# Kernel optimization log

Measured on AMD Instinct MI355X. Metric: run time of the kernel, lower is better.

Reference implementation:

```python
import jax, jax.numpy as jnp
import numpy as np

B, C, H, W = 4, 32, 64, 64
K = 3
HEADS = 8
SF = 4
D = C * K * K          # 288, unfold token dim
E = D // 2             # 144, reduced dim
DH = E // HEADS        # 18, head dim
SCALE = DH ** -0.5
N = H * W              # 4096 tokens


def unfold(x):
    # x: (B,C,H,W) -> (B, C*K*K, H*W), torch.nn.Unfold ordering (c, kh, kw)
    xp = jnp.pad(x, ((0, 0), (0, 0), (1, 1), (1, 1)))
    patches = jnp.stack([xp[:, :, i:i + H, j:j + W] for i in range(K) for j in range(K)], axis=2)
    return patches.reshape(x.shape[0], C * K * K, H * W)


def fold(cols):
    # inverse of unfold: scatter-add overlapping patches back, crop padding
    b = cols.shape[0]
    y = cols.reshape(b, C, K, K, H, W)
    out = jnp.zeros((b, C, H + 2, W + 2), cols.dtype)
    for i in range(K):
        for j in range(K):
            out = out.at[:, :, i:i + H, j:j + W].add(y[:, :, i, j])
    return out[:, :, 1:-1, 1:-1]


def layernorm_cols(cols, g, b):
    # LayerNorm over D applied on (B,N,D) view, returned as (B,D,N)
    xt = cols.transpose(0, 2, 1)
    mu = xt.mean(-1, keepdims=True)
    var = xt.var(-1, keepdims=True)
    y = (xt - mu) / jnp.sqrt(var + 1e-5) * g + b
    return y.transpose(0, 2, 1)


def emha(x, wr, br, wqkv, we, be):
    # x: (B, D, N)
    b, _, n_tok = x.shape
    xr = jnp.einsum('bdn,ed->ben', x, wr) + br[None, :, None]   # Conv1d k=1 reduction
    t = xr.transpose(0, 2, 1)                                   # (B,N,E)
    qkv = t @ wqkv.T                                            # Linear, no bias
    q, k, v = jnp.split(qkv, 3, axis=-1)
    n = n_tok // SF

    def rs(a):
        return a.reshape(b, n_tok, HEADS, DH).transpose(0, 2, 1, 3).reshape(b, HEADS, SF, n, DH)

    q, k, v = rs(q), rs(k), rs(v)
    attn = jax.nn.softmax(jnp.einsum('bhsnd,bhsmd->bhsnm', q, k) * SCALE, axis=-1)
    o = jnp.einsum('bhsnm,bhsmd->bhsnd', attn, v)
    o = o.reshape(b, HEADS, n_tok, DH).transpose(0, 2, 1, 3).reshape(b, n_tok, E).transpose(0, 2, 1)
    return jnp.einsum('ben,fe->bfn', o, we) + be[None, :, None]  # Conv1d k=1 expansion


def conv3x3(x, w, b):
    y = jax.lax.conv_general_dilated(x, w, (1, 1), ((1, 1), (1, 1)),
                                     dimension_numbers=('NCHW', 'OIHW', 'NCHW'))
    return y + b[None, :, None, None]


def setup_inputs() -> dict:
    key = jax.random.key(0)
    ks = jax.random.split(key, 20)
    s = 0.02
    inp = {
        'x': jax.random.normal(ks[0], (B, C, H, W), jnp.float32),
        'ln_g': jnp.ones((D,), jnp.float32),
        'ln_b': jnp.zeros((D,), jnp.float32),
        'conv_w': jax.random.normal(ks[1], (C, C, 3, 3), jnp.float32) * s,
        'conv_b': jnp.zeros((C,), jnp.float32),
    }
    for i in range(3):
        k0, k1, k2 = jax.random.split(ks[2 + i], 3)
        inp[f'wr{i+1}'] = jax.random.normal(k0, (E, D), jnp.float32) * s
        inp[f'br{i+1}'] = jnp.zeros((E,), jnp.float32)
        inp[f'wqkv{i+1}'] = jax.random.normal(k1, (3 * E, E), jnp.float32) * s
        inp[f'we{i+1}'] = jax.random.normal(k2, (D, E), jnp.float32) * s
        inp[f'be{i+1}'] = jnp.zeros((D,), jnp.float32)
    return inp


def reference(x, ln_g, ln_b, conv_w, conv_b,
              wr1, br1, wqkv1, we1, be1,
              wr2, br2, wqkv2, we2, be2,
              wr3, br3, wqkv3, we3, be3):
    t = x
    for (wr, br, wqkv, we, be) in ((wr1, br1, wqkv1, we1, be1),
                                   (wr2, br2, wqkv2, we2, be2),
                                   (wr3, br3, wqkv3, we3, be3)):
        cols = unfold(t)
        cols_n = layernorm_cols(cols, ln_g, ln_b)
        cols = emha(cols_n, wr, br, wqkv, we, be) + cols
        t = fold(cols)
    return x + jax.nn.elu(conv3x3(t, conv_w, conv_b))
```

## Files before the change

### kernel.cpp

```cpp
#include <hip/hip_runtime.h>
#include <math.h>

#define BN 4
#define CC 32
#define HH 64
#define WW 64
#define DD 288
#define EE 144
#define NTOK 4096
#define SCALE_F 0.2357022603955158f
#define QSCALE  0.3401074286f
#define QKST 384
#define MQKV 528

typedef __bf16 bf16x8 __attribute__((ext_vector_type(8)));
typedef float floatx4 __attribute__((ext_vector_type(4)));
typedef unsigned short u16x8 __attribute__((ext_vector_type(8)));

__device__ __forceinline__ unsigned short f2bf(float x) {
    unsigned int u = __float_as_uint(x);
    u += 0x7fffu + ((u >> 16) & 1u);
    return (unsigned short)(u >> 16);
}
__device__ __forceinline__ float bf2f(unsigned short s) {
    return __uint_as_float(((unsigned int)s) << 16);
}
__device__ __forceinline__ unsigned int pack_bf_trunc(float a, float b) {
    return __builtin_amdgcn_perm(__float_as_uint(b), __float_as_uint(a), 0x07060302u);
}

__global__ void precompute_k(const float* __restrict__ wr0, const float* __restrict__ br0,
                             const float* __restrict__ wr1, const float* __restrict__ br1,
                             const float* __restrict__ wr2, const float* __restrict__ br2,
                             const float* __restrict__ g,  const float* __restrict__ lb,
                             unsigned short* __restrict__ wg_bf, float* __restrict__ wgsum,
                             float* __restrict__ wbeta)
{
    int l = blockIdx.x;
    int e = threadIdx.x;
    const float* wr = (l == 0) ? wr0 : ((l == 1) ? wr1 : wr2);
    const float* br = (l == 0) ? br0 : ((l == 1) ? br1 : br2);
    float sg = 0.f, sb = 0.f;
    for (int d = 0; d < DD; ++d) {
        float w = wr[e * DD + d];
        float wgv = w * g[d];
        wg_bf[((size_t)l * EE + e) * DD + d] = f2bf(wgv);
        sg += wgv;
        sb += w * lb[d];
    }
    wgsum[l * EE + e] = sg;
    wbeta[l * EE + e] = sb + br[e];
}

__global__ __launch_bounds__(256) void convw_k(
    const float* __restrict__ wqkv0, const float* __restrict__ wqkv1, const float* __restrict__ wqkv2,
    const float* __restrict__ we0,   const float* __restrict__ we1,   const float* __restrict__ we2,
    unsigned short* __restrict__ wqkv_bf, unsigned short* __restrict__ we_bf)
{
    int idx = blockIdx.x * 256 + threadIdx.x;
    const int T1 = 3 * MQKV * 160;
    const int T2 = 3 * 288 * 160;
    if (idx < T1) {
        int l = idx / (MQKV * 160), r = idx % (MQKV * 160);
        int m = r / 160, k = r % 160;
        const float* w = (l == 0) ? wqkv0 : ((l == 1) ? wqkv1 : wqkv2);
        float v = 0.f;
        if (k < 144) {
            if (m < 192) {
                int h = m / 24, j = m % 24;
                if (j < 18) v = w[(h * 18 + j) * 144 + k] * QSCALE;
            } else if (m < 384) {
                int mm = m - 192, h = mm / 24, j = mm % 24;
                if (j < 18) v = w[(144 + h * 18 + j) * 144 + k];
            } else {
                v = w[(288 + (m - 384)) * 144 + k];
            }
        }
        wqkv_bf[idx] = f2bf(v);
    } else if (idx < T1 + T2) {
        int j = idx - T1;
        int l = j / (288 * 160), r = j % (288 * 160);
        int m = r / 160, k = r % 160;
        const float* w = (l == 0) ? we0 : ((l == 1) ? we1 : we2);
        we_bf[j] = (k < 144) ? f2bf(w[m * 144 + k]) : 0;
    }
}

__global__ __launch_bounds__(256) void unfold_k(const float* __restrict__ t,
    unsigned short* __restrict__ colsT,
    float* __restrict__ mu, float* __restrict__ rstd)
{
    __shared__ float red1[4][64], red2[4][64];
    int tid = threadIdx.x;
    int lane = tid & 63, cpart = tid >> 6;
    int b = blockIdx.x >> 6, nc = blockIdx.x & 63;
    int n = nc * 64 + lane;
    int h = n >> 6, w = n & 63;
    const float* tb = t + (size_t)b * CC * HH * WW;
    unsigned short loc[72];
    float s1 = 0.f, s2 = 0.f;
    #pragma unroll
    for (int c8 = 0; c8 < 8; ++c8) {
        int c = cpart * 8 + c8;
        const float* tc = tb + (size_t)c * 4096;
        #pragma unroll
        for (int i = 0; i < 3; ++i) {
            int hr = h + i - 1;
            bool rok = ((unsigned)hr < 64u);
            #pragma unroll
            for (int j = 0; j < 3; ++j) {
                int wc = w + j - 1;
                bool ok = rok && ((unsigned)wc < 64u);
                float v = ok ? tc[hr * 64 + wc] : 0.f;
                loc[c8 * 9 + i * 3 + j] = f2bf(v);
                s1 += v;
                s2 = fmaf(v, v, s2);
            }
        }
    }
    unsigned short* ct = colsT + ((size_t)b * NTOK + n) * 288 + cpart * 72;
    #pragma unroll
    for (int u = 0; u < 9; ++u)
        *(u16x8*)&ct[u * 8] = *(const u16x8*)&loc[u * 8];
    red1[cpart][lane] = s1;
    red2[cpart][lane] = s2;
    __syncthreads();
    if (tid < 64) {
        float a = red1[0][tid] + red1[1][tid] + red1[2][tid] + red1[3][tid];
        float q = red2[0][tid] + red2[1][tid] + red2[2][tid] + red2[3][tid];
        float m = a * (1.f / 288.f);
        float var = q * (1.f / 288.f) - m * m;
        int nn = nc * 64 + tid;
        mu[b * NTOK + nn] = m;
        rstd[b * NTOK + nn] = rsqrtf(var + 1e-5f);
    }
}

template<int K, int MODE, int NYB>
__global__ __launch_bounds__(256) void mgemm_k(
    const unsigned short* __restrict__ A, const unsigned short* __restrict__ Bt, int BST,
    unsigned short* __restrict__ Ct, unsigned short* __restrict__ Cv,
    const float* __restrict__ mu, const float* __restrict__ rstd,
    const float* __restrict__ wgsum, const float* __restrict__ wbeta,
    const float* __restrict__ bias)
{
    constexpr int NT = 64;
    __shared__ unsigned short Ts[64 * 56];
    int flat = blockIdx.x;
    int g  = (flat / (8 * NYB)) * 8 + (flat & 7);
    int jm = (flat % (8 * NYB)) >> 3;
    int n0 = (g & 63) * NT;
    int bI = g >> 6;
    int m0 = jm * 48;
    int tid = threadIdx.x;
    int wv = tid >> 6, lane = tid & 63;
    int l15 = lane & 15, l4 = lane >> 4;

    const unsigned short* Arow = A + (size_t)(m0 + l15) * K + l4 * 8;
    const unsigned short* Brow = Bt + ((size_t)bI * NTOK + n0 + wv * 16 + l15) * BST + l4 * 8;

    floatx4 acc[3];
    acc[0] = acc[1] = acc[2] = (floatx4){0.f, 0.f, 0.f, 0.f};

    #pragma unroll
    for (int ks = 0; ks < K / 32; ++ks) {
        bf16x8 bfr = *(const bf16x8*)(Brow + ks * 32);
        #pragma unroll
        for (int mi = 0; mi < 3; ++mi) {
            bf16x8 af = *(const bf16x8*)(Arow + (size_t)mi * 16 * K + ks * 32);
            acc[mi] = __builtin_amdgcn_mfma_f32_16x16x32_bf16(af, bfr, acc[mi], 0, 0, 0);
        }
    }

    int n_l = wv * 16 + l15;

    if (MODE == 2) {
        #pragma unroll
        for (int mi = 0; mi < 3; ++mi)
            #pragma unroll
            for (int r = 0; r < 4; ++r) {
                int m_l = mi * 16 + l4 * 4 + r;
                Ts[m_l * 72 + n_l] = f2bf(acc[mi][r] + bias[m0 + m_l]);
            }
        __syncthreads();
        for (int u = tid; u < 48 * 8; u += 256) {
            int row = u >> 3, seg = u & 7;
            unsigned short* dst = Ct + ((size_t)bI * DD + m0 + row) * NTOK + n0 + seg * 8;
            *(u16x8*)dst = *(const u16x8*)&Ts[row * 72 + seg * 8];
        }
    } else {
        bool vpath = (MODE == 0) && (m0 >= 384);
        float muv = 0.f, rsv = 0.f;
        if (MODE == 1) {
            int n_g = n0 + n_l;
            muv = mu[bI * NTOK + n_g];
            rsv = rstd[bI * NTOK + n_g];
        }
        #pragma unroll
        for (int mi = 0; mi < 3; ++mi)
            #pragma unroll
            for (int r = 0; r < 4; ++r) {
                int m_l = mi * 16 + l4 * 4 + r;
                float v = acc[mi][r];
                if (MODE == 1) v = rsv * (v - muv * wgsum[m0 + m_l]) + wbeta[m0 + m_l];
                if (!vpath) Ts[n_l * 56 + m_l] = f2bf(v);
                else        Ts[m_l * 72 + n_l] = f2bf(v);
            }
        __syncthreads();
        if (!vpath) {
            const int CTS = (MODE == 1) ? 160 : QKST;
            if (tid < 128) {
                int row = tid >> 1, half = tid & 1;
                unsigned short* dst = Ct + ((size_t)bI * NTOK + n0 + row) * CTS + m0 + half * 24;
                const unsigned short* src = &Ts[row * 56 + half * 24];
                #pragma unroll
                for (int u = 0; u < 3; ++u)
                    *(u16x8*)&dst[u * 8] = *(const u16x8*)&src[u * 8];
                if (MODE == 1 && m0 == 96) {
                    u16x8 z = (u16x8)0;
                    *(u16x8*)(Ct + ((size_t)bI * NTOK + n0 + row) * 160 + 144 + half * 8) = z;
                }
            }
        } else {
            for (int u = tid; u < 48 * 8; u += 256) {
                int row = u >> 3, seg = u & 7;
                unsigned short* dst = Cv + ((size_t)bI * EE + (m0 - 384) + row) * NTOK + n0 + seg * 8;
                *(u16x8*)dst = *(const u16x8*)&Ts[row * 72 + seg * 8];
            }
        }
    }
}

__global__ __launch_bounds__(256) void attn_k2(const unsigned short* __restrict__ qkT,
                                               const unsigned short* __restrict__ vF,
                                               unsigned short* __restrict__ oT)
{
    __shared__ unsigned short Ks[128 * 40];
    __shared__ unsigned short Vs[32 * 136];
    __shared__ unsigned short Ps[4 * 32 * 72];

    int blk = blockIdx.x;
    int bhs = blk & 127;
    int qc  = blk >> 7;
    int b = bhs >> 5, h = (bhs >> 2) & 7, s = bhs & 3;
    int tid  = threadIdx.x;
    int wv   = tid >> 6;
    int lane = tid & 63;
    int l15 = lane & 15, l4 = lane >> 4;
    int q0 = qc * 128;
    int tokbase = s * 1024;

    const unsigned short* qkb = qkT + (size_t)b * NTOK * QKST;

    if (tid < 128) {
        u16x8 z = (u16x8)0;
        *(u16x8*)&Ks[tid * 40 + 24] = z;
    } else {
        for (int v = tid - 128; v < 14 * 16; v += 128) {
            int d = 18 + (v >> 4), seg = v & 15;
            unsigned short val = (d == 31) ? (unsigned short)0x3F80 : (unsigned short)0;
            u16x8 vv = (u16x8)val;
            *(u16x8*)&Vs[d * 136 + seg * 8] = vv;
        }
    }

    bf16x8 qf[2];
    #pragma unroll
    for (int ni = 0; ni < 2; ++ni) {
        u16x8 raw = *(const u16x8*)(qkb + (size_t)(tokbase + q0 + wv * 32 + ni * 16 + l15) * QKST
                                    + 24 * h + l4 * 8);
        if (l4 == 3) raw = (u16x8)0;
        qf[ni] = *(bf16x8*)&raw;
    }

    floatx4 oacc[2][2];
    #pragma unroll
    for (int i = 0; i < 2; ++i)
        #pragma unroll
        for (int j = 0; j < 2; ++j)
            oacc[i][j] = (floatx4){0.f, 0.f, 0.f, 0.f};

    unsigned short* Pw = &Ps[wv * 32 * 72];

    u16x8 preg[3];
    int vb = tid - 128;
    bool v3 = (vb < 32);
    if (tid < 128) {
        const unsigned short* src = qkb + (size_t)(tokbase + tid) * QKST + 192 + 24 * h;
        preg[0] = *(const u16x8*)&src[0];
        preg[1] = *(const u16x8*)&src[8];
        preg[2] = *(const u16x8*)&src[16];
    } else {
        const unsigned short* vbb = vF + (size_t)b * EE * NTOK + tokbase;
        #pragma unroll
        for (int u = 0; u < 3; ++u) {
            int idx = vb + u * 128;
            if (u < 2 || v3) {
                int d = idx >> 4, seg = idx & 15;
                preg[u] = *(const u16x8*)(vbb + (size_t)(h * 18 + d) * NTOK + seg * 8);
            }
        }
    }

    for (int c0 = 0; c0 < 1024; c0 += 128) {
        __syncthreads();
        if (tid < 128) {
            unsigned short* dk = &Ks[tid * 40];
            *(u16x8*)&dk[0]  = preg[0];
            *(u16x8*)&dk[8]  = preg[1];
            *(u16x8*)&dk[16] = preg[2];
        } else {
            #pragma unroll
            for (int u = 0; u < 3; ++u) {
                int idx = vb + u * 128;
                if (u < 2 || v3) {
                    int d = idx >> 4, seg = idx & 15;
                    *(u16x8*)&Vs[d * 136 + seg * 8] = preg[u];
                }
            }
        }
        int cn = c0 + 128;
        if (cn < 1024) {
            if (tid < 128) {
                const unsigned short* src = qkb + (size_t)(tokbase + cn + tid) * QKST + 192 + 24 * h;
                preg[0] = *(const u16x8*)&src[0];
                preg[1] = *(const u16x8*)&src[8];
                preg[2] = *(const u16x8*)&src[16];
            } else {
                const unsigned short* vbb = vF + (size_t)b * EE * NTOK + tokbase + cn;
                #pragma unroll
                for (int u = 0; u < 3; ++u) {
                    int idx = vb + u * 128;
                    if (u < 2 || v3) {
                        int d = idx >> 4, seg = idx & 15;
                        preg[u] = *(const u16x8*)(vbb + (size_t)(h * 18 + d) * NTOK + seg * 8);
                    }
                }
            }
        }
        __syncthreads();

        #pragma unroll
        for (int sub = 0; sub < 2; ++sub) {
            bf16x8 kf[4];
            #pragma unroll
            for (int mi = 0; mi < 4; ++mi)
                kf[mi] = *(const bf16x8*)&Ks[(sub * 64 + mi * 16 + l15) * 40 + l4 * 8];

            floatx4 sacc[4][2];
            #pragma unroll
            for (int mi = 0; mi < 4; ++mi)
                #pragma unroll
                for (int ni = 0; ni < 2; ++ni) {
                    floatx4 z = (floatx4){0.f, 0.f, 0.f, 0.f};
                    sacc[mi][ni] = __builtin_amdgcn_mfma_f32_16x16x32_bf16(kf[mi], qf[ni], z, 0, 0, 0);
                }

            #pragma unroll
            for (int mi = 0; mi < 4; ++mi)
                #pragma unroll
                for (int ni = 0; ni < 2; ++ni) {
                    int ql   = ni * 16 + l15;
                    int tokb = mi * 16 + l4 * 4;
                    unsigned int lo = pack_bf_trunc(exp2f(sacc[mi][ni][0]), exp2f(sacc[mi][ni][1]));
                    unsigned int hi = pack_bf_trunc(exp2f(sacc[mi][ni][2]), exp2f(sacc[mi][ni][3]));
                    uint2 pk = make_uint2(lo, hi);
                    *(uint2*)&Pw[ql * 72 + tokb] = pk;
                }

            #pragma unroll
            for (int ks = 0; ks < 2; ++ks) {
                bf16x8 pf[2], vf[2];
                pf[0] = *(const bf16x8*)&Pw[(     l15) * 72 + ks * 32 + l4 * 8];
                pf[1] = *(const bf16x8*)&Pw[(16 + l15) * 72 + ks * 32 + l4 * 8];
                vf[0] = *(const bf16x8*)&Vs[(     l15) * 136 + sub * 64 + ks * 32 + l4 * 8];
                vf[1] = *(const bf16x8*)&Vs[(16 + l15) * 136 + sub * 64 + ks * 32 + l4 * 8];
                #pragma unroll
                for (int mi = 0; mi < 2; ++mi)
                    #pragma unroll
                    for (int nd = 0; nd < 2; ++nd)
                        oacc[mi][nd] = __builtin_amdgcn_mfma_f32_16x16x32_bf16(pf[mi], vf[nd], oacc[mi][nd], 0, 0, 0);
            }
        }
    }

    float* fO = (float*)Pw;
    #pragma unroll
    for (int mi = 0; mi < 2; ++mi)
        #pragma unroll
        for (int r = 0; r < 4; ++r) {
            float lsum = __shfl(oacc[mi][1][r], (lane & 48) | 15, 64);
            float inv  = 1.f / lsum;
            int ql = mi * 16 + l4 * 4 + r;
            fO[ql * 33 + l15] = oacc[mi][0][r] * inv;
            if (l15 < 2) fO[ql * 33 + 16 + l15] = oacc[mi][1][r] * inv;
        }

    {
        int q = lane & 31, dh = lane >> 5;
        size_t rowi = (size_t)b * NTOK + tokbase + q0 + wv * 32 + q;
        unsigned short* orow = oT + rowi * 160 + h * 18;
        for (int i = dh; i < 9; i += 2) {
            float a  = fO[q * 33 + 2 * i];
            float bb = fO[q * 33 + 2 * i + 1];
            *(unsigned int*)&orow[2 * i] = (unsigned)f2bf(a) | ((unsigned)f2bf(bb) << 16);
        }
        if (h == 7) {
            u16x8 z = (u16x8)0;
            *(u16x8*)(oT + rowi * 160 + 144 + dh * 8) = z;
        }
    }
}

__global__ __launch_bounds__(256) void fold_k(const unsigned short* __restrict__ cols,
                                              const float* __restrict__ tprev,
                                              float* __restrict__ t)
{
    int idx = blockIdx.x * 256 + threadIdx.x;
    int w = idx & 63;
    int h = (idx >> 6) & 63;
    int c = (idx >> 12) & 31;
    int b = idx >> 17;
    const unsigned short* cb = cols + (size_t)b * DD * NTOK + (size_t)c * 9 * NTOK;
    float sum = 0.f;
    #pragma unroll
    for (int i = 0; i < 3; ++i) {
        int hs = h + 1 - i;
        if ((unsigned)hs < 64u) {
            #pragma unroll
            for (int j = 0; j < 3; ++j) {
                int ws_ = w + 1 - j;
                if ((unsigned)ws_ < 64u)
                    sum += bf2f(cb[(size_t)(i * 3 + j) * NTOK + hs * 64 + ws_]);
            }
        }
    }
    int ch = (h == 0 || h == 63) ? 2 : 3;
    int cw_ = (w == 0 || w == 63) ? 2 : 3;
    t[idx] = sum + (float)(ch * cw_) * tprev[idx];
}

__global__ __launch_bounds__(256) void conv_k(const float* __restrict__ t,
    const float* __restrict__ cw, const float* __restrict__ cbias,
    const float* __restrict__ x, float* __restrict__ out)
{
    __shared__ float wsh[CC * 9];
    int blk = blockIdx.x;
    int band = blk & 3, co = (blk >> 2) & 31, b = blk >> 7;
    int tid = threadIdx.x;
    for (int u = tid; u < CC * 9; u += 256) wsh[u] = cw[co * CC * 9 + u];
    __syncthreads();
    int h = band * 16 + (tid >> 4);
    int w0 = (tid & 15) << 2;
    const float* tb = t + (size_t)b * CC * 4096;
    float bias = cbias[co];
    float a0 = bias, a1 = bias, a2 = bias, a3 = bias;
    for (int ci = 0; ci < CC; ++ci) {
        const float* tc = tb + (size_t)ci * 4096;
        const float* wr = &wsh[ci * 9];
        #pragma unroll
        for (int i = 0; i < 3; ++i) {
            int hr = h + i - 1;
            if ((unsigned)hr < 64u) {
                const float* row = tc + hr * 64;
                float vl = (w0 > 0)  ? row[w0 - 1] : 0.f;
                float4 c4 = *(const float4*)&row[w0];
                float vr = (w0 < 60) ? row[w0 + 4] : 0.f;
                float wj0 = wr[i * 3], wj1 = wr[i * 3 + 1], wj2 = wr[i * 3 + 2];
                a0 = fmaf(wj0, vl,   a0); a0 = fmaf(wj1, c4.x, a0); a0 = fmaf(wj2, c4.y, a0);
                a1 = fmaf(wj0, c4.x, a1); a1 = fmaf(wj1, c4.y, a1); a1 = fmaf(wj2, c4.z, a1);
                a2 = fmaf(wj0, c4.y, a2); a2 = fmaf(wj1, c4.z, a2); a2 = fmaf(wj2, c4.w, a2);
                a3 = fmaf(wj0, c4.z, a3); a3 = fmaf(wj1, c4.w, a3); a3 = fmaf(wj2, vr,   a3);
            }
        }
    }
    size_t oidx = ((size_t)(b * CC + co) * 4096) + h * 64 + w0;
    float4 xin = *(const float4*)&x[oidx];
    float4 o;
    o.x = xin.x + ((a0 > 0.f) ? a0 : (__expf(a0) - 1.f));
    o.y = xin.y + ((a1 > 0.f) ? a1 : (__expf(a1) - 1.f));
    o.z = xin.z + ((a2 > 0.f) ? a2 : (__expf(a2) - 1.f));
    o.w = xin.w + ((a3 > 0.f) ? a3 : (__expf(a3) - 1.f));
    *(float4*)&out[oidx] = o;
}

extern "C" void kernel_launch(void* const* d_in, const int* in_sizes, int n_in,
                              void* d_out, int out_size, void* d_ws, size_t ws_size,
                              hipStream_t stream)
{
    const float* x    = (const float*)d_in[0];
    const float* ln_g = (const float*)d_in[1];
    const float* ln_b = (const float*)d_in[2];
    const float* cw   = (const float*)d_in[3];
    const float* cb   = (const float*)d_in[4];
    const float* wr[3]   = {(const float*)d_in[5],  (const float*)d_in[10], (const float*)d_in[15]};
    const float* br[3]   = {(const float*)d_in[6],  (const float*)d_in[11], (const float*)d_in[16]};
    const float* wqkv[3] = {(const float*)d_in[7],  (const float*)d_in[12], (const float*)d_in[17]};
    const float* we[3]   = {(const float*)d_in[8],  (const float*)d_in[13], (const float*)d_in[18]};
    const float* be[3]   = {(const float*)d_in[9],  (const float*)d_in[14], (const float*)d_in[19]};
    float* out = (float*)d_out;

    char* p = (char*)d_ws;
    unsigned short* cols_bf = (unsigned short*)p; p += (size_t)BN * DD * NTOK * 2;
    unsigned short* colsT = (unsigned short*)p; p += (size_t)BN * NTOK * 288 * 2;
    unsigned short* oT = colsT;
    unsigned short* xrT   = (unsigned short*)p; p += (size_t)BN * NTOK * 160 * 2;
    unsigned short* qkT   = (unsigned short*)p; p += (size_t)BN * NTOK * QKST * 2;
    unsigned short* vF    = (unsigned short*)p; p += (size_t)BN * EE * NTOK * 2;
    float* mu   = (float*)p;              p += (size_t)BN * NTOK * 4;
    float* rstd = (float*)p;              p += (size_t)BN * NTOK * 4;
    float* tA   = (float*)p;              p += (size_t)BN * CC * HH * WW * 4;
    float* tB   = (float*)p;              p += (size_t)BN * CC * HH * WW * 4;
    unsigned short* wg_bf   = (unsigned short*)p; p += (size_t)3 * EE * DD * 2;
    unsigned short* wqkv_bf = (unsigned short*)p; p += (size_t)3 * MQKV * 160 * 2;
    unsigned short* we_bf   = (unsigned short*)p; p += (size_t)3 * DD * 160 * 2;
    float* wgsum = (float*)p;             p += 3 * EE * 4;
    float* wbeta = (float*)p;             p += 3 * EE * 4;
    (void)in_sizes; (void)n_in; (void)out_size; (void)ws_size;

    precompute_k<<<3, 144, 0, stream>>>(wr[0], br[0], wr[1], br[1], wr[2], br[2],
                                        ln_g, ln_b, wg_bf, wgsum, wbeta);
    convw_k<<<1530, 256, 0, stream>>>(wqkv[0], wqkv[1], wqkv[2], we[0], we[1], we[2],
                                      wqkv_bf, we_bf);

    const float* tin = x;
    float* touts[3] = {tA, tB, tA};
    for (int l = 0; l < 3; ++l) {
        unfold_k<<<256, 256, 0, stream>>>(tin, colsT, mu, rstd);
        mgemm_k<288, 1, 3><<<768, 256, 0, stream>>>(
            wg_bf + (size_t)l * EE * DD, colsT, 288, xrT, nullptr,
            mu, rstd, wgsum + l * EE, wbeta + l * EE, nullptr);
        mgemm_k<160, 0, 11><<<2816, 256, 0, stream>>>(
            wqkv_bf + (size_t)l * MQKV * 160, xrT, 160, qkT, vF,
            nullptr, nullptr, nullptr, nullptr, nullptr);
        attn_k2<<<1024, 256, 0, stream>>>(qkT, vF, oT);
        mgemm_k<160, 2, 6><<<1536, 256, 0, stream>>>(
            we_bf + (size_t)l * DD * 160, oT, 160, cols_bf, nullptr,
            nullptr, nullptr, nullptr, nullptr, be[l]);
        fold_k<<<2048, 256, 0, stream>>>(cols_bf, tin, touts[l]);
        tin = touts[l];
    }
    conv_k<<<512, 256, 0, stream>>>(tA, cw, cb, x, out);
}
```

Baseline: 445.7 us.

## Fuse fold with next unfold/layernorm stats and final fold with conv

Merges the two weight-setup kernels into one launch. Fuses the fold of each layer with the following unfold and LayerNorm statistics, so each block rebuilds three rows of the folded image in shared memory and emits the transposed columns directly. The last fold is fused into the 3x3 conv plus ELU epilogue, so the final t tensor is never written out. This cuts kernel launches and global round trips, but the fold work for halo rows is recomputed three times and the fused kernels run only 256 blocks, which may underfill the GPU.

```diff
diff --git a/kernel.cpp b/kernel.cpp
--- a/kernel.cpp
+++ b/kernel.cpp
@@ -29,35 +29,37 @@
     return __builtin_amdgcn_perm(__float_as_uint(b), __float_as_uint(a), 0x07060302u);
 }
 
-__global__ void precompute_k(const float* __restrict__ wr0, const float* __restrict__ br0,
-                             const float* __restrict__ wr1, const float* __restrict__ br1,
-                             const float* __restrict__ wr2, const float* __restrict__ br2,
-                             const float* __restrict__ g,  const float* __restrict__ lb,
-                             unsigned short* __restrict__ wg_bf, float* __restrict__ wgsum,
-                             float* __restrict__ wbeta)
-{
-    int l = blockIdx.x;
-    int e = threadIdx.x;
-    const float* wr = (l == 0) ? wr0 : ((l == 1) ? wr1 : wr2);
-    const float* br = (l == 0) ? br0 : ((l == 1) ? br1 : br2);
-    float sg = 0.f, sb = 0.f;
-    for (int d = 0; d < DD; ++d) {
-        float w = wr[e * DD + d];
-        float wgv = w * g[d];
-        wg_bf[((size_t)l * EE + e) * DD + d] = f2bf(wgv);
-        sg += wgv;
-        sb += w * lb[d];
-    }
-    wgsum[l * EE + e] = sg;
-    wbeta[l * EE + e] = sb + br[e];
-}
-
-__global__ __launch_bounds__(256) void convw_k(
+__global__ __launch_bounds__(256) void setup_k(
+    const float* __restrict__ wr0, const float* __restrict__ br0,
+    const float* __restrict__ wr1, const float* __restrict__ br1,
+    const float* __restrict__ wr2, const float* __restrict__ br2,
+    const float* __restrict__ g,  const float* __restrict__ lb,
     const float* __restrict__ wqkv0, const float* __restrict__ wqkv1, const float* __restrict__ wqkv2,
     const float* __restrict__ we0,   const float* __restrict__ we1,   const float* __restrict__ we2,
+    unsigned short* __restrict__ wg_bf, float* __restrict__ wgsum, float* __restrict__ wbeta,
     unsigned short* __restrict__ wqkv_bf, unsigned short* __restrict__ we_bf)
 {
-    int idx = blockIdx.x * 256 + threadIdx.x;
+    int blk = blockIdx.x;
+    int tid = threadIdx.x;
+    if (blk < 3) {
+        if (tid < 144) {
+            int l = blk, e = tid;
+            const float* wr = (l == 0) ? wr0 : ((l == 1) ? wr1 : wr2);
+            const float* br = (l == 0) ? br0 : ((l == 1) ? br1 : br2);
+            float sg = 0.f, sb = 0.f;
+            for (int d = 0; d < DD; ++d) {
+                float w = wr[e * DD + d];
+                float wgv = w * g[d];
+                wg_bf[((size_t)l * EE + e) * DD + d] = f2bf(wgv);
+                sg += wgv;
+                sb += w * lb[d];
+            }
+            wgsum[l * EE + e] = sg;
+            wbeta[l * EE + e] = sb + br[e];
+        }
+        return;
+    }
+    int idx = (blk - 3) * 256 + tid;
     const int T1 = 3 * MQKV * 160;
     const int T2 = 3 * 288 * 160;
     if (idx < T1) {
@@ -133,6 +135,171 @@
         int nn = nc * 64 + tid;
         mu[b * NTOK + nn] = m;
         rstd[b * NTOK + nn] = rsqrtf(var + 1e-5f);
+    }
+}
+
+__global__ __launch_bounds__(256) void fu_k(const unsigned short* __restrict__ cols,
+                                            const float* __restrict__ tprev,
+                                            float* __restrict__ tout,
+                                            unsigned short* __restrict__ colsT,
+                                            float* __restrict__ mu, float* __restrict__ rstd)
+{
+    __shared__ float tl[3 * CC * 64];
+    __shared__ float red1[4][64], red2[4][64];
+    int tid = threadIdx.x;
+    int b = blockIdx.x >> 6, h = blockIdx.x & 63;
+    const unsigned short* cbb = cols + (size_t)b * DD * NTOK;
+    const float* tpb = tprev + (size_t)b * CC * 4096;
+    float* tob = tout + (size_t)b * CC * 4096;
+
+    #pragma unroll
+    for (int p = 0; p < 24; ++p) {
+        int idx = p * 256 + tid;
+        int w = idx & 63;
+        int rc = idx >> 6;
+        int c = rc & 31;
+        int r3 = rc >> 5;
+        int r = h + r3 - 1;
+        float val = 0.f;
+        if ((unsigned)r < 64u) {
+            const unsigned short* cc = cbb + (size_t)c * 9 * NTOK;
+            float sum = 0.f;
+            #pragma unroll
+            for (int i = 0; i < 3; ++i) {
+                int rs = r + 1 - i;
+                if ((unsigned)rs < 64u) {
+                    #pragma unroll
+                    for (int j = 0; j < 3; ++j) {
+                        int ws = w + 1 - j;
+                        if ((unsigned)ws < 64u)
+                            sum += bf2f(cc[(size_t)(i * 3 + j) * NTOK + rs * 64 + ws]);
+                    }
+                }
+            }
+            int ch = (r == 0 || r == 63) ? 2 : 3;
+            int cw_ = (w == 0 || w == 63) ? 2 : 3;
+            val = sum + (float)(ch * cw_) * tpb[(size_t)c * 4096 + r * 64 + w];
+            if (r3 == 1) tob[(size_t)c * 4096 + r * 64 + w] = val;
+        }
+        tl[idx] = val;
+    }
+    __syncthreads();
+
+    int lane = tid & 63, cpart = tid >> 6;
+    int w = lane;
+    int n = h * 64 + w;
+    unsigned short loc[72];
+    float s1 = 0.f, s2 = 0.f;
+    #pragma unroll
+    for (int c8 = 0; c8 < 8; ++c8) {
+        int c = cpart * 8 + c8;
+        #pragma unroll
+        for (int i = 0; i < 3; ++i) {
+            const float* row = &tl[(i * 32 + c) * 64];
+            #pragma unroll
+            for (int j = 0; j < 3; ++j) {
+                int wc = w + j - 1;
+                float v = ((unsigned)wc < 64u) ? row[wc] : 0.f;
+                loc[c8 * 9 + i * 3 + j] = f2bf(v);
+                s1 += v;
+                s2 = fmaf(v, v, s2);
+            }
+        }
+    }
+    unsigned short* ct = colsT + ((size_t)b * NTOK + n) * 288 + cpart * 72;
+    #pragma unroll
+    for (int u = 0; u < 9; ++u)
+        *(u16x8*)&ct[u * 8] = *(const u16x8*)&loc[u * 8];
+    red1[cpart][lane] = s1;
+    red2[cpart][lane] = s2;
+    __syncthreads();
+    if (tid < 64) {
+        float a = red1[0][tid] + red1[1][tid] + red1[2][tid] + red1[3][tid];
+        float q = red2[0][tid] + red2[1][tid] + red2[2][tid] + red2[3][tid];
+        float m = a * (1.f / 288.f);
+        float var = q * (1.f / 288.f) - m * m;
+        mu[b * NTOK + h * 64 + tid] = m;
+        rstd[b * NTOK + h * 64 + tid] = rsqrtf(var + 1e-5f);
+    }
+}
+
+__global__ __launch_bounds__(256) void foldconv_k(const unsigned short* __restrict__ cols,
+    const float* __restrict__ tprev,
+    const float* __restrict__ cw, const float* __restrict__ cbias,
+    const float* __restrict__ x, float* __restrict__ out)
+{
+    __shared__ float tl[3 * CC * 64];
+    int tid = threadIdx.x;
+    int b = blockIdx.x >> 6, h = blockIdx.x & 63;
+    const unsigned short* cbb = cols + (size_t)b * DD * NTOK;
+    const float* tpb = tprev + (size_t)b * CC * 4096;
+
+    #pragma unroll
+    for (int p = 0; p < 24; ++p) {
+        int idx = p * 256 + tid;
+        int w = idx & 63;
+        int rc = idx >> 6;
+        int c = rc & 31;
+        int r3 = rc >> 5;
+        int r = h + r3 - 1;
+        float val = 0.f;
+        if ((unsigned)r < 64u) {
+            const unsigned short* cc = cbb + (size_t)c * 9 * NTOK;
+            float sum = 0.f;
+            #pragma unroll
+            for (int i = 0; i < 3; ++i) {
+                int rs = r + 1 - i;
+                if ((unsigned)rs < 64u) {
+                    #pragma unroll
+                    for (int j = 0; j < 3; ++j) {
+                        int ws = w + 1 - j;
+                        if ((unsigned)ws < 64u)
+                            sum += bf2f(cc[(size_t)(i * 3 + j) * NTOK + rs * 64 + ws]);
+                    }
+                }
+            }
+            int ch = (r == 0 || r == 63) ? 2 : 3;
+            int cw_ = (w == 0 || w == 63) ? 2 : 3;
+            val = sum + (float)(ch * cw_) * tpb[(size_t)c * 4096 + r * 64 + w];
+        }
+        tl[idx] = val;
+    }
+    __syncthreads();
+
+    int co = tid >> 3;
+    int w0 = (tid & 7) * 8;
+    float acc[8];
+    float bias = cbias[co];
+    #pragma unroll
+    for (int k = 0; k < 8; ++k) acc[k] = bias;
+    const float* wco = cw + co * CC * 9;
+    for (int ci = 0; ci < CC; ++ci) {
+        const float* wrow = wco + ci * 9;
+        #pragma unroll
+        for (int i = 0; i < 3; ++i) {
+            const float* row = &tl[(i * 32 + ci) * 64];
+            float w0v = wrow[i * 3], w1v = wrow[i * 3 + 1], w2v = wrow[i * 3 + 2];
+            float vl = (w0 > 0)  ? row[w0 - 1] : 0.f;
+            float vr = (w0 < 56) ? row[w0 + 8] : 0.f;
+            float c0 = row[w0], c1 = row[w0 + 1], c2 = row[w0 + 2], c3 = row[w0 + 3];
+            float c4 = row[w0 + 4], c5 = row[w0 + 5], c6 = row[w0 + 6], c7 = row[w0 + 7];
+            acc[0] = fmaf(w0v, vl, acc[0]); acc[0] = fmaf(w1v, c0, acc[0]); acc[0] = fmaf(w2v, c1, acc[0]);
+            acc[1] = fmaf(w0v, c0, acc[1]); acc[1] = fmaf(w1v, c1, acc[1]); acc[1] = fmaf(w2v, c2, acc[1]);
+            acc[2] = fmaf(w0v, c1, acc[2]); acc[2] = fmaf(w1v, c2, acc[2]); acc[2] = fmaf(w2v, c3, acc[2]);
+            acc[3] = fmaf(w0v, c2, acc[3]); acc[3] = fmaf(w1v, c3, acc[3]); acc[3] = fmaf(w2v, c4, acc[3]);
+            acc[4] = fmaf(w0v, c3, acc[4]); acc[4] = fmaf(w1v, c4, acc[4]); acc[4] = fmaf(w2v, c5, acc[4]);
+            acc[5] = fmaf(w0v, c4, acc[5]); acc[5] = fmaf(w1v, c5, acc[5]); acc[5] = fmaf(w2v, c6, acc[5]);
+            acc[6] = fmaf(w0v, c5, acc[6]); acc[6] = fmaf(w1v, c6, acc[6]); acc[6] = fmaf(w2v, c7, acc[6]);
+            acc[7] = fmaf(w0v, c6, acc[7]); acc[7] = fmaf(w1v, c7, acc[7]); acc[7] = fmaf(w2v, vr, acc[7]);
+        }
+    }
+    size_t oidx = ((size_t)(b * CC + co) * 4096) + h * 64 + w0;
+    const float* xin = &x[oidx];
+    float* op = &out[oidx];
+    #pragma unroll
+    for (int k = 0; k < 8; ++k) {
+        float e = (acc[k] > 0.f) ? acc[k] : (__expf(acc[k]) - 1.f);
+        op[k] = xin[k] + e;
     }
 }
 
@@ -412,78 +579,6 @@
     }
 }
 
-__global__ __launch_bounds__(256) void fold_k(const unsigned short* __restrict__ cols,
-                                              const float* __restrict__ tprev,
-                                              float* __restrict__ t)
-{
-    int idx = blockIdx.x * 256 + threadIdx.x;
-    int w = idx & 63;
-    int h = (idx >> 6) & 63;
-    int c = (idx >> 12) & 31;
-    int b = idx >> 17;
-    const unsigned short* cb = cols + (size_t)b * DD * NTOK + (size_t)c * 9 * NTOK;
-    float sum = 0.f;
-    #pragma unroll
-    for (int i = 0; i < 3; ++i) {
-        int hs = h + 1 - i;
-        if ((unsigned)hs < 64u) {
-            #pragma unroll
-            for (int j = 0; j < 3; ++j) {
-                int ws_ = w + 1 - j;
-                if ((unsigned)ws_ < 64u)
-                    sum += bf2f(cb[(size_t)(i * 3 + j) * NTOK + hs * 64 + ws_]);
-            }
-        }
-    }
-    int ch = (h == 0 || h == 63) ? 2 : 3;
-    int cw_ = (w == 0 || w == 63) ? 2 : 3;
-    t[idx] = sum + (float)(ch * cw_) * tprev[idx];
-}
-
-__global__ __launch_bounds__(256) void conv_k(const float* __restrict__ t,
-    const float* __restrict__ cw, const float* __restrict__ cbias,
-    const float* __restrict__ x, float* __restrict__ out)
-{
-    __shared__ float wsh[CC * 9];
-    int blk = blockIdx.x;
-    int band = blk & 3, co = (blk >> 2) & 31, b = blk >> 7;
-    int tid = threadIdx.x;
-    for (int u = tid; u < CC * 9; u += 256) wsh[u] = cw[co * CC * 9 + u];
-    __syncthreads();
-    int h = band * 16 + (tid >> 4);
-    int w0 = (tid & 15) << 2;
-    const float* tb = t + (size_t)b * CC * 4096;
-    float bias = cbias[co];
-    float a0 = bias, a1 = bias, a2 = bias, a3 = bias;
-    for (int ci = 0; ci < CC; ++ci) {
-        const float* tc = tb + (size_t)ci * 4096;
-        const float* wr = &wsh[ci * 9];
-        #pragma unroll
-        for (int i = 0; i < 3; ++i) {
-            int hr = h + i - 1;
-            if ((unsigned)hr < 64u) {
-                const float* row = tc + hr * 64;
-                float vl = (w0 > 0)  ? row[w0 - 1] : 0.f;
-                float4 c4 = *(const float4*)&row[w0];
-                float vr = (w0 < 60) ? row[w0 + 4] : 0.f;
-                float wj0 = wr[i * 3], wj1 = wr[i * 3 + 1], wj2 = wr[i * 3 + 2];
-                a0 = fmaf(wj0, vl,   a0); a0 = fmaf(wj1, c4.x, a0); a0 = fmaf(wj2, c4.y, a0);
-                a1 = fmaf(wj0, c4.x, a1); a1 = fmaf(wj1, c4.y, a1); a1 = fmaf(wj2, c4.z, a1);
-                a2 = fmaf(wj0, c4.y, a2); a2 = fmaf(wj1, c4.z, a2); a2 = fmaf(wj2, c4.w, a2);
-                a3 = fmaf(wj0, c4.z, a3); a3 = fmaf(wj1, c4.w, a3); a3 = fmaf(wj2, vr,   a3);
-            }
-        }
-    }
-    size_t oidx = ((size_t)(b * CC + co) * 4096) + h * 64 + w0;
-    float4 xin = *(const float4*)&x[oidx];
-    float4 o;
-    o.x = xin.x + ((a0 > 0.f) ? a0 : (__expf(a0) - 1.f));
-    o.y = xin.y + ((a1 > 0.f) ? a1 : (__expf(a1) - 1.f));
-    o.z = xin.z + ((a2 > 0.f) ? a2 : (__expf(a2) - 1.f));
-    o.w = xin.w + ((a3 > 0.f) ? a3 : (__expf(a3) - 1.f));
-    *(float4*)&out[oidx] = o;
-}
-
 extern "C" void kernel_launch(void* const* d_in, const int* in_sizes, int n_in,
                               void* d_out, int out_size, void* d_ws, size_t ws_size,
                               hipStream_t stream)
@@ -518,15 +613,14 @@
     float* wbeta = (float*)p;             p += 3 * EE * 4;
     (void)in_sizes; (void)n_in; (void)out_size; (void)ws_size;
 
-    precompute_k<<<3, 144, 0, stream>>>(wr[0], br[0], wr[1], br[1], wr[2], br[2],
-                                        ln_g, ln_b, wg_bf, wgsum, wbeta);
-    convw_k<<<1530, 256, 0, stream>>>(wqkv[0], wqkv[1], wqkv[2], we[0], we[1], we[2],
-                                      wqkv_bf, we_bf);
-
-    const float* tin = x;
-    float* touts[3] = {tA, tB, tA};
+    setup_k<<<1533, 256, 0, stream>>>(wr[0], br[0], wr[1], br[1], wr[2], br[2], ln_g, ln_b,
+                                      wqkv[0], wqkv[1], wqkv[2], we[0], we[1], we[2],
+                                      wg_bf, wgsum, wbeta, wqkv_bf, we_bf);
+
+    const float* tprevs[3] = {x, tA, tB};
+    float* touts[3] = {tA, tB, nullptr};
+    unfold_k<<<256, 256, 0, stream>>>(x, colsT, mu, rstd);
     for (int l = 0; l < 3; ++l) {
-        unfold_k<<<256, 256, 0, stream>>>(tin, colsT, mu, rstd);
         mgemm_k<288, 1, 3><<<768, 256, 0, stream>>>(
             wg_bf + (size_t)l * EE * DD, colsT, 288, xrT, nullptr,
             mu, rstd, wgsum + l * EE, wbeta + l * EE, nullptr);
@@ -537,8 +631,10 @@
         mgemm_k<160, 2, 6><<<1536, 256, 0, stream>>>(
             we_bf + (size_t)l * DD * 160, oT, 160, cols_bf, nullptr,
             nullptr, nullptr, nullptr, nullptr, be[l]);
-        fold_k<<<2048, 256, 0, stream>>>(cols_bf, tin, touts[l]);
-        tin = touts[l];
-    }
-    conv_k<<<512, 256, 0, stream>>>(tA, cw, cb, x, out);
-}
+        if (l < 2) {
+            fu_k<<<256, 256, 0, stream>>>(cols_bf, tprevs[l], touts[l], colsT, mu, rstd);
+        } else {
+            foldconv_k<<<256, 256, 0, stream>>>(cols_bf, tprevs[2], cw, cb, x, out);
+        }
+    }
+}
```

Measured after the change: 591.2 us. 1.33x slower.
